# Performance work log

Hardware: AMD Instinct MI355X
Metric: run time of the kernel (lower is better)

## Reference

```python
import math
import jax, jax.numpy as jnp
import numpy as np

B = 8          # number of graphs in the batch
NMAX = 256     # max nodes per graph (padding size)
K = 128        # num_kernels
H = 32         # num_heads
NTYPE = 101    # max_node_type + 1


def setup_inputs() -> dict:
    key = jax.random.key(0)
    ks = jax.random.split(key, 10)
    sizes = np.asarray(NMAX - np.arange(B) * 16, dtype=np.int32)  # 256,240,...,144 -> ragged
    N = int(sizes.sum())  # 1600
    coord = jax.random.normal(ks[0], (N, 3), dtype=jnp.float32) * 3.0
    node_type = jax.random.randint(ks[1], (N,), 0, NTYPE, dtype=jnp.int32)
    gaussian_means = jax.random.uniform(ks[2], (1, K), minval=0.0, maxval=3.0, dtype=jnp.float32)
    gaussian_stds = jax.random.uniform(ks[3], (1, K), minval=0.0, maxval=3.0, dtype=jnp.float32)
    # nn.Embedding(max_node_type+1, 2) tables; original init is const(0)/const(1),
    # we perturb so the computation is non-degenerate.
    mul_w = jax.random.normal(ks[4], (NTYPE, 2), dtype=jnp.float32) * 0.1
    bias_w = 1.0 + jax.random.normal(ks[5], (NTYPE, 2), dtype=jnp.float32) * 0.1
    W1 = jax.random.normal(ks[6], (K, K), dtype=jnp.float32) / math.sqrt(K)
    b1 = jnp.zeros((K,), dtype=jnp.float32)
    W2 = jax.random.normal(ks[7], (K, H), dtype=jnp.float32) / math.sqrt(K)
    b2 = jnp.zeros((H,), dtype=jnp.float32)
    return {
        "coord": coord,
        "gaussian_means": gaussian_means,
        "gaussian_stds": gaussian_stds,
        "mul_w": mul_w,
        "bias_w": bias_w,
        "W1": W1,
        "b1": b1,
        "W2": W2,
        "b2": b2,
        "node_type": node_type,
        "batch_num_nodes": jnp.asarray(sizes),
    }


def reference(coord, gaussian_means, gaussian_stds, mul_w, bias_w, W1, b1, W2, b2,
              node_type, batch_num_nodes):
    N = coord.shape[0]
    offsets = jnp.concatenate([jnp.zeros((1,), dtype=batch_num_nodes.dtype),
                               jnp.cumsum(batch_num_nodes)[:-1]])
    ar = jnp.arange(NMAX)
    idx = offsets[:, None] + ar[None, :]                     # [B, n] flat node index per graph slot
    valid = ar[None, :] < batch_num_nodes[:, None]           # [B, n] node mask
    idx_c = jnp.clip(idx, 0, N - 1)
    pc = coord[idx_c]                                        # [B, n, 3] padded coords
    pt = node_type[idx_c]                                    # [B, n]

    # pairwise Euclidean distance (torch.cdist p=2), sqrt-safe at 0
    diff = pc[:, :, None, :] - pc[:, None, :, :]             # [B, n, n, 3]
    sq = jnp.sum(diff * diff, axis=-1)                       # [B, n, n]
    nz = sq > 0
    dist = jnp.where(nz, jnp.sqrt(jnp.where(nz, sq, 1.0)), 0.0)

    # outer-sum of per-node (src, dst) scaling embeddings
    mul_e = mul_w[pt]                                        # [B, n, 2]
    bias_e = bias_w[pt]
    mul = mul_e[:, :, None, 0] + mul_e[:, None, :, 1]        # [B, n, n]
    bias = bias_e[:, :, None, 0] + bias_e[:, None, :, 1]
    scaled = mul * dist + bias                               # [B, n, n]

    means = gaussian_means.reshape(-1)                       # [K]
    stds = jnp.abs(gaussian_stds.reshape(-1)) + 0.01         # [K]
    z = (scaled[..., None] - means) / stds                   # [B, n, n, K]
    gk = jnp.exp(-0.5 * z * z) / (-math.sqrt(2.0 * math.pi) * stds)

    h = jax.nn.gelu(gk @ W1 + b1, approximate=False)         # exact gelu like torch F.gelu
    out = h @ W2 + b2                                        # [B, n, n, H]

    pair = valid[:, :, None] & valid[:, None, :]             # padded positions -> -inf
    return jnp.where(pair[..., None], out, -jnp.inf)
```

## Files before the change

kernel.cpp:

```cpp
#include <hip/hip_runtime.h>
#include <math.h>

#define NMAXC 256
#define KC 128
#define HC 32
#define BC 8
#define TP 256
#define NEG_SENTINEL (-1.0e30f)
#define LOG2E 1.4426950408889634f

typedef __bf16 bf16x8 __attribute__((ext_vector_type(8)));
typedef float  f32x16 __attribute__((ext_vector_type(16)));
union FragU { uint4 u; bf16x8 v; };

#if __has_builtin(__builtin_amdgcn_exp2f)
#define EXP2F(x) __builtin_amdgcn_exp2f(x)
#else
#define EXP2F(x) exp2f(x)
#endif

__device__ __forceinline__ unsigned pack2(float lo, float hi) {
    return __builtin_amdgcn_perm(__float_as_uint(hi), __float_as_uint(lo), 0x07060302u);
}

__device__ __forceinline__ int swap23(int k) {
    return (k & ~12) | ((k & 4) << 1) | ((k & 8) >> 1);
}

__global__ __launch_bounds__(256) void se3d_prep(const float* __restrict__ W1,
                                                 const float* __restrict__ W2,
                                                 const float* __restrict__ gm,
                                                 const float* __restrict__ gs,
                                                 unsigned* __restrict__ wsu) {
    int t = blockIdx.x * 256 + threadIdx.x;
    if (t < 2048) {
        int fb = t >> 6, lane = t & 63;
        int nt = fb >> 3, ks = fb & 7;
        int n  = nt * 32 + (lane & 31);
        int k0 = ks * 16 + 8 * (lane >> 5);
        unsigned u[4];
#pragma unroll
        for (int p = 0; p < 4; ++p)
            u[p] = pack2(-W1[(k0 + 2 * p) * KC + n], -W1[(k0 + 2 * p + 1) * KC + n]);
        ((uint4*)wsu)[t] = make_uint4(u[0], u[1], u[2], u[3]);
    } else if (t < 2560) {
        int c = t - 2048;
        int ks = c >> 6, lane = c & 63;
        int n  = lane & 31;
        int k0 = ks * 16 + 8 * (lane >> 5);
        unsigned u[4];
#pragma unroll
        for (int p = 0; p < 4; ++p) {
            int ta = swap23(k0 + 2 * p);
            int tb = swap23(k0 + 2 * p + 1);
            u[p] = pack2(W2[ta * HC + n], W2[tb * HC + n]);
        }
        ((uint4*)wsu)[2048 + c] = make_uint4(u[0], u[1], u[2], u[3]);
    } else if (t < 2688) {
        int k = t - 2560;
        float inv = 1.0f / (fabsf(gs[k]) + 0.01f);
        float m  = gm[k];
        float A2 = -0.5f * inv * inv * LOG2E;
        float* wf = (float*)wsu + 10240;
        wf[2 * k]     = A2;
        wf[2 * k + 1] = -2.0f * A2 * m;
        wf[256 + k]   = A2 * m * m + log2f(0.3989422804014327f * inv);
    }
}

__global__ __launch_bounds__(256, 3) void se3d_main(
    const float* __restrict__ coord, const float* __restrict__ mulw,
    const float* __restrict__ biasw, const float* __restrict__ b1,
    const float* __restrict__ b2, const int* __restrict__ ntype,
    const int* __restrict__ bnn, const void* __restrict__ ws,
    float* __restrict__ out)
{
    __shared__ float scaled[TP];
    __shared__ int   obase[TP];
    __shared__ float cAB[2 * KC];
    __shared__ float cC[KC];

    const int b = blockIdx.y;
    const int n = bnn[b];
    const int q0 = blockIdx.x * TP;
    const int tid = threadIdx.x;

    if (q0 >= n * n) {
        int v = q0 + tid - n * n;
        int wdt = 256 - n;
        int na = n * wdt;
        int i, j;
        if (v < na) { i = v / wdt; j = n + (v - i * wdt); }
        else        { int vp = v - na; i = n + (vp >> 8); j = vp & 255; }
        float4 s4 = make_float4(NEG_SENTINEL, NEG_SENTINEL, NEG_SENTINEL, NEG_SENTINEL);
        float4* o = (float4*)(out + ((size_t)((b * NMAXC + i) * NMAXC + j)) * HC);
#pragma unroll
        for (int t = 0; t < 8; ++t) o[t] = s4;
        return;
    }

    int off = 0;
    for (int t = 0; t < b; ++t) off += bnn[t];

    const float* wf = (const float*)((const char*)ws + 40960);
    cAB[tid] = wf[tid];
    if (tid < KC) cC[tid] = wf[256 + tid];
    {
        int q = q0 + tid;
        int i = q / n;
        int j = q - i * n;
        int gi = off + i, gj = off + j;
        float dx = coord[gi * 3 + 0] - coord[gj * 3 + 0];
        float dy = coord[gi * 3 + 1] - coord[gj * 3 + 1];
        float dz = coord[gi * 3 + 2] - coord[gj * 3 + 2];
        float sq = dx * dx + dy * dy + dz * dz;
        float dist = sq > 0.f ? sqrtf(sq) : 0.f;
        int ti = ntype[gi], tj = ntype[gj];
        scaled[tid] = (mulw[ti * 2 + 0] + mulw[tj * 2 + 1]) * dist
                    + (biasw[ti * 2 + 0] + biasw[tj * 2 + 1]);
        obase[tid]  = ((b * NMAXC + i) * NMAXC + j) * HC;
    }
    __syncthreads();

    const int l = tid & 63, w = tid >> 6;
    const int hi = l >> 5, ln31 = l & 31;
    const int m0 = w * 64;
    const float sA = scaled[m0 + ln31];
    const float sB = scaled[m0 + 32 + ln31];

    const bf16x8* wsW1 = (const bf16x8*)ws;
    const bf16x8* wsW2 = (const bf16x8*)((const char*)ws + 32768);

    FragU gfrA[8], gfrB[8];
#pragma unroll
    for (int ks = 0; ks < 8; ++ks) {
        int k0 = ks * 16 + 8 * hi;
        const float4* ab = (const float4*)(cAB + 2 * k0);
        const float4* cc = (const float4*)(cC + k0);
        float4 ab0 = ab[0], ab1 = ab[1], ab2 = ab[2], ab3 = ab[3];
        float4 c0 = cc[0], c1 = cc[1];
#pragma unroll
        for (int grp = 0; grp < 2; ++grp) {
            float s = grp ? sB : sA;
            float t0 = EXP2F(fmaf(fmaf(ab0.x, s, ab0.y), s, c0.x));
            float t1 = EXP2F(fmaf(fmaf(ab0.z, s, ab0.w), s, c0.y));
            float t2 = EXP2F(fmaf(fmaf(ab1.x, s, ab1.y), s, c0.z));
            float t3 = EXP2F(fmaf(fmaf(ab1.z, s, ab1.w), s, c0.w));
            float t4 = EXP2F(fmaf(fmaf(ab2.x, s, ab2.y), s, c1.x));
            float t5 = EXP2F(fmaf(fmaf(ab2.z, s, ab2.w), s, c1.y));
            float t6 = EXP2F(fmaf(fmaf(ab3.x, s, ab3.y), s, c1.z));
            float t7 = EXP2F(fmaf(fmaf(ab3.z, s, ab3.w), s, c1.w));
            FragU& g = grp ? gfrB[ks] : gfrA[ks];
            g.u.x = pack2(t0, t1);
            g.u.y = pack2(t2, t3);
            g.u.z = pack2(t4, t5);
            g.u.w = pack2(t6, t7);
        }
    }

    const float KSG = -1.702f * LOG2E;
    f32x16 c2A, c2B;
#pragma unroll
    for (int g = 0; g < 4; ++g) {
        float4 t4 = *(const float4*)(b2 + 8 * g + 4 * hi);
        c2A[4 * g + 0] = t4.x; c2A[4 * g + 1] = t4.y;
        c2A[4 * g + 2] = t4.z; c2A[4 * g + 3] = t4.w;
        c2B[4 * g + 0] = t4.x; c2B[4 * g + 1] = t4.y;
        c2B[4 * g + 2] = t4.z; c2B[4 * g + 3] = t4.w;
    }

#define GELU_PACK(AA, F0, F1) do {                                      \
    float vv[16];                                                       \
    _Pragma("unroll")                                                   \
    for (int r = 0; r < 16; ++r) {                                      \
        float x = AA[r];                                                \
        float e = EXP2F(x * KSG);                                       \
        vv[r] = x * __builtin_amdgcn_rcpf(1.0f + e);                    \
    }                                                                   \
    F0.u.x = pack2(vv[0],  vv[1]);  F0.u.y = pack2(vv[2],  vv[3]);      \
    F0.u.z = pack2(vv[4],  vv[5]);  F0.u.w = pack2(vv[6],  vv[7]);      \
    F1.u.x = pack2(vv[8],  vv[9]);  F1.u.y = pack2(vv[10], vv[11]);     \
    F1.u.z = pack2(vv[12], vv[13]); F1.u.w = pack2(vv[14], vv[15]);     \
} while (0)

#pragma unroll
    for (int nt = 0; nt < 4; ++nt) {
        f32x16 aA, aB;
#pragma unroll
        for (int g = 0; g < 4; ++g) {
            float4 t4 = *(const float4*)(b1 + nt * 32 + 8 * g + 4 * hi);
            aA[4 * g + 0] = t4.x; aA[4 * g + 1] = t4.y;
            aA[4 * g + 2] = t4.z; aA[4 * g + 3] = t4.w;
            aB[4 * g + 0] = t4.x; aB[4 * g + 1] = t4.y;
            aB[4 * g + 2] = t4.z; aB[4 * g + 3] = t4.w;
        }
#pragma unroll
        for (int ks = 0; ks < 8; ++ks) {
            bf16x8 w0 = wsW1[(nt * 8 + ks) * 64 + l];
            aA = __builtin_amdgcn_mfma_f32_32x32x16_bf16(w0, gfrA[ks].v, aA, 0, 0, 0);
            aB = __builtin_amdgcn_mfma_f32_32x32x16_bf16(w0, gfrB[ks].v, aB, 0, 0, 0);
        }
        FragU fA0, fA1, fB0, fB1;
        GELU_PACK(aA, fA0, fA1);
        GELU_PACK(aB, fB0, fB1);
        bf16x8 u0 = wsW2[(2 * nt + 0) * 64 + l];
        bf16x8 u1 = wsW2[(2 * nt + 1) * 64 + l];
        c2A = __builtin_amdgcn_mfma_f32_32x32x16_bf16(u0, fA0.v, c2A, 0, 0, 0);
        c2A = __builtin_amdgcn_mfma_f32_32x32x16_bf16(u1, fA1.v, c2A, 0, 0, 0);
        c2B = __builtin_amdgcn_mfma_f32_32x32x16_bf16(u0, fB0.v, c2B, 0, 0, 0);
        c2B = __builtin_amdgcn_mfma_f32_32x32x16_bf16(u1, fB1.v, c2B, 0, 0, 0);
    }
#undef GELU_PACK

    {
        const int obA = obase[m0 + ln31];
        float* opA = out + (size_t)obA + 4 * hi;
#pragma unroll
        for (int g = 0; g < 4; ++g)
            *(float4*)(opA + 8 * g) =
                make_float4(c2A[4 * g], c2A[4 * g + 1], c2A[4 * g + 2], c2A[4 * g + 3]);
        const int obB = obase[m0 + 32 + ln31];
        float* opB = out + (size_t)obB + 4 * hi;
#pragma unroll
        for (int g = 0; g < 4; ++g)
            *(float4*)(opB + 8 * g) =
                make_float4(c2B[4 * g], c2B[4 * g + 1], c2B[4 * g + 2], c2B[4 * g + 3]);
    }
}

extern "C" void kernel_launch(void* const* d_in, const int* in_sizes, int n_in,
                              void* d_out, int out_size, void* d_ws, size_t ws_size,
                              hipStream_t stream) {
    const float* coord = (const float*)d_in[0];
    const float* gm    = (const float*)d_in[1];
    const float* gs    = (const float*)d_in[2];
    const float* mulw  = (const float*)d_in[3];
    const float* biasw = (const float*)d_in[4];
    const float* W1    = (const float*)d_in[5];
    const float* b1    = (const float*)d_in[6];
    const float* W2    = (const float*)d_in[7];
    const float* b2    = (const float*)d_in[8];
    const int* ntype   = (const int*)d_in[9];
    const int* bnn     = (const int*)d_in[10];
    float* out = (float*)d_out;

    hipLaunchKernelGGL(se3d_prep, dim3(11), dim3(256), 0, stream,
                       W1, W2, gm, gs, (unsigned*)d_ws);
    hipLaunchKernelGGL(se3d_main, dim3(NMAXC * NMAXC / TP, BC), dim3(256),
                       0, stream,
                       coord, mulw, biasw, b1, b2, ntype, bnn, d_ws, out);
}
```

Baseline: 121.7 us.

## Stage packed weights in LDS via async global_load_lds and precompute offsets

Each block now copies the pre-packed bf16 W1/W2 fragments (40 KB) into shared memory with asynchronous global-to-LDS loads, and the MFMA loops read their weights from LDS instead of global memory. The prep kernel also precomputes per-graph node offsets and a magic-multiplier reciprocal, so the main kernel skips its serial prefix-sum loop and replaces the integer divide with a multiply-shift. The extra 40 KB of LDS per block may reduce the number of resident blocks per CU, and this change adds no explicit wait on the async loads before their first use.

Result: faster. 117.2 us, median of 2 (-3.7%).

```diff
diff --git a/kernel.cpp b/kernel.cpp
--- a/kernel.cpp
+++ b/kernel.cpp
@@ -31,6 +31,7 @@
                                                  const float* __restrict__ W2,
                                                  const float* __restrict__ gm,
                                                  const float* __restrict__ gs,
+                                                 const int* __restrict__ bnn,
                                                  unsigned* __restrict__ wsu) {
     int t = blockIdx.x * 256 + threadIdx.x;
     if (t < 2048) {
@@ -65,6 +66,15 @@
         wf[2 * k]     = A2;
         wf[2 * k + 1] = -2.0f * A2 * m;
         wf[256 + k]   = A2 * m * m + log2f(0.3989422804014327f * inv);
+    } else if (t < 2696) {
+        int g = t - 2688;
+        int o = 0;
+        for (int i = 0; i < g; ++i) o += bnn[i];
+        ((int*)wsu)[10624 + g] = o;
+    } else if (t < 2704) {
+        int g = t - 2696;
+        unsigned n = (unsigned)bnn[g];
+        wsu[10632 + g] = (1u << 25) / n + 1u;
     }
 }
 
@@ -75,6 +85,7 @@
     const int* __restrict__ bnn, const void* __restrict__ ws,
     float* __restrict__ out)
 {
+    __shared__ __attribute__((aligned(16))) uint4 ldsW[2560];
     __shared__ float scaled[TP];
     __shared__ int   obase[TP];
     __shared__ float cAB[2 * KC];
@@ -99,15 +110,25 @@
         return;
     }
 
-    int off = 0;
-    for (int t = 0; t < b; ++t) off += bnn[t];
+    const int l = tid & 63, w = tid >> 6;
+
+#pragma unroll
+    for (int t = 0; t < 10; ++t) {
+        int chunk = w * 10 + t;
+        __builtin_amdgcn_global_load_lds(
+            (const uint4*)ws + chunk * 64 + l,
+            &ldsW[chunk * 64], 16, 0, 0);
+    }
+
+    const int      off = ((const int*)ws)[10624 + b];
+    const unsigned mg  = ((const unsigned*)ws)[10632 + b];
 
     const float* wf = (const float*)((const char*)ws + 40960);
-    cAB[tid] = wf[tid];
+    cAB[tid < 256 ? tid : 0] = wf[tid < 256 ? tid : 0];
     if (tid < KC) cC[tid] = wf[256 + tid];
     {
         int q = q0 + tid;
-        int i = q / n;
+        int i = (int)(((unsigned long long)(unsigned)q * mg) >> 25);
         int j = q - i * n;
         int gi = off + i, gj = off + j;
         float dx = coord[gi * 3 + 0] - coord[gj * 3 + 0];
@@ -122,14 +143,13 @@
     }
     __syncthreads();
 
-    const int l = tid & 63, w = tid >> 6;
     const int hi = l >> 5, ln31 = l & 31;
     const int m0 = w * 64;
     const float sA = scaled[m0 + ln31];
     const float sB = scaled[m0 + 32 + ln31];
 
-    const bf16x8* wsW1 = (const bf16x8*)ws;
-    const bf16x8* wsW2 = (const bf16x8*)((const char*)ws + 32768);
+    const bf16x8* wsW1 = (const bf16x8*)ldsW;
+    const bf16x8* wsW2 = (const bf16x8*)ldsW + 2048;
 
     FragU gfrA[8], gfrB[8];
 #pragma unroll
@@ -245,7 +265,7 @@
     float* out = (float*)d_out;
 
     hipLaunchKernelGGL(se3d_prep, dim3(11), dim3(256), 0, stream,
-                       W1, W2, gm, gs, (unsigned*)d_ws);
+                       W1, W2, gm, gs, bnn, (unsigned*)d_ws);
     hipLaunchKernelGGL(se3d_main, dim3(NMAXC * NMAXC / TP, BC), dim3(256),
                        0, stream,
                        coord, mulw, biasw, b1, b2, ntype, bnn, d_ws, out);
```
